# Kernel optimization log

Hardware: AMD Instinct MI355X
Metric: run time of the kernel (lower is better)

## Reference

```python
import jax, jax.numpy as jnp
import numpy as np

SHIFT = 4
MARGIN = 0.15


def _shift_loss(f1, m1, f2, m2):
    # f1,f2: [B,C,H,W] float; m1,m2: [B,1,H,W] bool
    # Original repeats masks to C channels; broadcasting is equivalent,
    # but mask.sum over (1,2,3) then includes a factor of C.
    C = f1.shape[1]
    dists = []
    for i in range(2 * SHIFT + 1):
        off = -SHIFT + i
        f2r = jnp.roll(f2, off, axis=-1)
        m2r = jnp.roll(m2, off, axis=-1)
        mask = m1 & m2r                              # [B,1,H,W]
        diff = jnp.where(mask, f1 - f2r, 0.0)        # broadcast over C
        num = jnp.sum(diff * diff, axis=(1, 2, 3))   # ||.||_2^2
        den = C * jnp.sum(mask, axis=(1, 2, 3)).astype(f1.dtype) + 0.001
        dists.append(num / den)
    return jnp.min(jnp.stack(dists, axis=0), axis=0)  # min over 9 shifts -> [B]


def setup_inputs() -> dict:
    key = jax.random.key(0)
    ka, kp, kn, kma, kmp, kmn = jax.random.split(key, 6)
    B, C, H, W = 64, 16, 32, 512
    a = jax.random.normal(ka, (B, C, H, W), dtype=jnp.float32)
    p = jax.random.normal(kp, (B, C, H, W), dtype=jnp.float32)
    n = jax.random.normal(kn, (B, C, H, W), dtype=jnp.float32)
    ma = jax.random.bernoulli(kma, 0.8, (B, 1, H, W))
    mp = jax.random.bernoulli(kmp, 0.8, (B, 1, H, W))
    mn = jax.random.bernoulli(kmn, 0.8, (B, 1, H, W))
    return {"a": a, "p": p, "n": n, "ma": ma, "mp": mp, "mn": mn}


def reference(a, p, n, ma, mp, mn):
    ap_loss = _shift_loss(a, ma, p, mp)
    an_loss = _shift_loss(a, ma, n, mn)
    loss = jax.nn.relu(ap_loss - an_loss + MARGIN)
    return jnp.mean(loss)
```

## Files before the change

### kernel.cpp

```cpp
#include <hip/hip_runtime.h>

#define NB 64
#define NC 16
#define NH 32
#define NW 512
#define HW (NH * NW)
#define CHW (NC * HW)
#define NOFF 9

#define WS_NUM_AP 0
#define WS_NUM_AN 576
#define WS_CNT_AP 1152
#define WS_CNT_AN 1728
#define WS_FLOATS 2304

__device__ __forceinline__ float wave_sum_f(float v) {
#pragma unroll
    for (int o = 32; o > 0; o >>= 1) v += __shfl_down(v, o, 64);
    return v;
}

__global__ __launch_bounds__(256, 4) void num_kernel(
    const float* __restrict__ a, const float* __restrict__ p,
    const float* __restrict__ n, const int* __restrict__ ma,
    const int* __restrict__ mp, const int* __restrict__ mn,
    float* __restrict__ ws)
{
    const int b    = blockIdx.z;
    const int pair = blockIdx.y & 1;
    const int cg   = blockIdx.y >> 1;
    const int tid  = blockIdx.x * 256 + threadIdx.x;
    const int pos0 = tid * 4;
    const int w0   = pos0 & (NW - 1);
    const int row  = pos0 - w0;
    const int idxm = row + ((w0 - 4) & (NW - 1));
    const int idxp = row + ((w0 + 4) & (NW - 1));

    const int* MA = ma + b * HW;
    const int* M2 = (pair ? mn : mp) + b * HW;
    int4 mav = *(const int4*)(MA + pos0);
    int4 mf0 = *(const int4*)(M2 + idxm);
    int4 mf1 = *(const int4*)(M2 + pos0);
    int4 mf2 = *(const int4*)(M2 + idxp);

    float m1f[4]  = {mav.x ? 1.f : 0.f, mav.y ? 1.f : 0.f,
                     mav.z ? 1.f : 0.f, mav.w ? 1.f : 0.f};
    float m2f[12] = {mf0.x ? 1.f : 0.f, mf0.y ? 1.f : 0.f, mf0.z ? 1.f : 0.f, mf0.w ? 1.f : 0.f,
                     mf1.x ? 1.f : 0.f, mf1.y ? 1.f : 0.f, mf1.z ? 1.f : 0.f, mf1.w ? 1.f : 0.f,
                     mf2.x ? 1.f : 0.f, mf2.y ? 1.f : 0.f, mf2.z ? 1.f : 0.f, mf2.w ? 1.f : 0.f};

    const float* A = a + (size_t)b * CHW + (size_t)cg * 8 * HW;
    const float* F = (pair ? n : p) + (size_t)b * CHW + (size_t)cg * 8 * HW;

    float sa2[4];
    float sf2[12];
    float crS[NOFF];
#pragma unroll
    for (int j = 0; j < 4; ++j) sa2[j] = 0.f;
#pragma unroll
    for (int k = 0; k < 12; ++k) sf2[k] = 0.f;
#pragma unroll
    for (int s = 0; s < NOFF; ++s) crS[s] = 0.f;

#pragma unroll 2
    for (int c = 0; c < 8; ++c) {
        const float* Ac = A + c * HW;
        const float* Fc = F + c * HW;

        float4 av4 = *(const float4*)(Ac + pos0);
        float fb[12];
        *(float4*)&fb[0] = *(const float4*)(Fc + idxm);
        *(float4*)&fb[4] = *(const float4*)(Fc + pos0);
        *(float4*)&fb[8] = *(const float4*)(Fc + idxp);
        float avr[4] = {av4.x, av4.y, av4.z, av4.w};

        float am[4], fm[12];
#pragma unroll
        for (int j = 0; j < 4; ++j) am[j] = avr[j] * m1f[j];
#pragma unroll
        for (int k = 0; k < 12; ++k) fm[k] = fb[k] * m2f[k];

#pragma unroll
        for (int j = 0; j < 4; ++j) sa2[j] = fmaf(am[j], am[j], sa2[j]);
#pragma unroll
        for (int k = 0; k < 12; ++k) sf2[k] = fmaf(fm[k], fm[k], sf2[k]);
#pragma unroll
        for (int s = 0; s < NOFF; ++s) {
#pragma unroll
            for (int j = 0; j < 4; ++j) {
                crS[s] = fmaf(am[j], fm[j + 8 - s], crS[s]);
            }
        }
    }

    float sx[NOFF], cxf[NOFF];
#pragma unroll
    for (int s = 0; s < NOFF; ++s) {
        float t = 0.f, cc = 0.f;
#pragma unroll
        for (int j = 0; j < 4; ++j) {
            const int k = j + 8 - s;
            t  = fmaf(m2f[k], sa2[j], t);
            t  = fmaf(m1f[j], sf2[k], t);
            cc = fmaf(m1f[j], m2f[k], cc);
        }
        sx[s]  = fmaf(-2.f, crS[s], t);
        cxf[s] = cc;
    }

    __shared__ float red[4][20];
    const int lane = threadIdx.x & 63;
    const int wid  = threadIdx.x >> 6;

#pragma unroll
    for (int s = 0; s < NOFF; ++s) sx[s] = wave_sum_f(sx[s]);
    if (cg == 0) {
#pragma unroll
        for (int s = 0; s < NOFF; ++s) cxf[s] = wave_sum_f(cxf[s]);
    }
    if (lane == 0) {
#pragma unroll
        for (int s = 0; s < NOFF; ++s) {
            red[wid][s] = sx[s];
            red[wid][9 + s] = cxf[s];
        }
    }
    __syncthreads();

    float* numws = ws + (pair ? WS_NUM_AN : WS_NUM_AP) + b * NOFF;
    float* cntws = ws + (pair ? WS_CNT_AN : WS_CNT_AP) + b * NOFF;
    const int i = threadIdx.x;
    if (i < 9) {
        float v = red[0][i] + red[1][i] + red[2][i] + red[3][i];
        atomicAdd(numws + i, v);
    } else if (i < 18 && cg == 0) {
        float v = red[0][i] + red[1][i] + red[2][i] + red[3][i];
        atomicAdd(cntws + (i - 9), v);
    }
}

__global__ void finish_kernel(const float* __restrict__ ws, float* __restrict__ out)
{
    const int b = threadIdx.x;
    const float* num_ap = ws + WS_NUM_AP;
    const float* num_an = ws + WS_NUM_AN;
    const float* cnt_ap = ws + WS_CNT_AP;
    const float* cnt_an = ws + WS_CNT_AN;

    float ap = 3.4e38f, an = 3.4e38f;
#pragma unroll
    for (int s = 0; s < NOFF; ++s) {
        ap = fminf(ap, num_ap[b * NOFF + s] / (16.f * cnt_ap[b * NOFF + s] + 0.001f));
        an = fminf(an, num_an[b * NOFF + s] / (16.f * cnt_an[b * NOFF + s] + 0.001f));
    }
    float loss = fmaxf(ap - an + 0.15f, 0.f);
    loss = wave_sum_f(loss);
    if (b == 0) out[0] = loss * (1.0f / 64.f);
}

extern "C" void kernel_launch(void* const* d_in, const int* in_sizes, int n_in,
                              void* d_out, int out_size, void* d_ws, size_t ws_size,
                              hipStream_t stream) {
    const float* a = (const float*)d_in[0];
    const float* p = (const float*)d_in[1];
    const float* n = (const float*)d_in[2];
    const int* ma = (const int*)d_in[3];
    const int* mp = (const int*)d_in[4];
    const int* mn = (const int*)d_in[5];
    float* ws = (float*)d_ws;
    float* out = (float*)d_out;

    hipMemsetAsync(d_ws, 0, WS_FLOATS * sizeof(float), stream);

    num_kernel<<<dim3(16, 4, NB), 256, 0, stream>>>(a, p, n, ma, mp, mn, ws);
    finish_kernel<<<1, 64, 0, stream>>>(ws, out);
}
```

Baseline: 212.9 us.

## Stage shifted feature rows through LDS with double-buffered async global-to-LDS loads

```diff
diff --git a/kernel.cpp b/kernel.cpp
--- a/kernel.cpp
+++ b/kernel.cpp
@@ -18,6 +18,13 @@
 #pragma unroll
     for (int o = 32; o > 0; o >>= 1) v += __shfl_down(v, o, 64);
     return v;
+}
+
+__device__ __forceinline__ void stage16(const float* g, float* lds) {
+    __builtin_amdgcn_global_load_lds(
+        (const __attribute__((address_space(1))) void*)g,
+        (__attribute__((address_space(3))) void*)lds,
+        16, 0, 0);
 }
 
 __global__ __launch_bounds__(256, 4) void num_kernel(
@@ -29,12 +36,17 @@
     const int b    = blockIdx.z;
     const int pair = blockIdx.y & 1;
     const int cg   = blockIdx.y >> 1;
-    const int tid  = blockIdx.x * 256 + threadIdx.x;
-    const int pos0 = tid * 4;
-    const int w0   = pos0 & (NW - 1);
-    const int row  = pos0 - w0;
-    const int idxm = row + ((w0 - 4) & (NW - 1));
-    const int idxp = row + ((w0 + 4) & (NW - 1));
+    const int lane = threadIdx.x & 63;
+    const int wid  = threadIdx.x >> 6;
+
+    const int blockStart = blockIdx.x * 1024;
+    const int lp   = threadIdx.x * 4;
+    const int lrow = lp & ~(NW - 1);
+    const int lw   = lp & (NW - 1);
+    const int pos0 = blockStart + lp;
+    const int grow = pos0 - lw;
+    const int idxm = grow + ((lw - 4) & (NW - 1));
+    const int idxp = grow + ((lw + 4) & (NW - 1));
 
     const int* MA = ma + b * HW;
     const int* M2 = (pair ? mn : mp) + b * HW;
@@ -51,6 +63,11 @@
 
     const float* A = a + (size_t)b * CHW + (size_t)cg * 8 * HW;
     const float* F = (pair ? n : p) + (size_t)b * CHW + (size_t)cg * 8 * HW;
+    const float* AG = A + blockStart;
+    const float* FG = F + blockStart;
+
+    __shared__ float fbuf[2][2][1024];
+    __shared__ float red[4][20];
 
     float sa2[4];
     float sf2[12];
@@ -62,33 +79,53 @@
 #pragma unroll
     for (int s = 0; s < NOFF; ++s) crS[s] = 0.f;
 
-#pragma unroll 2
-    for (int c = 0; c < 8; ++c) {
-        const float* Ac = A + c * HW;
-        const float* Fc = F + c * HW;
-
-        float4 av4 = *(const float4*)(Ac + pos0);
-        float fb[12];
-        *(float4*)&fb[0] = *(const float4*)(Fc + idxm);
-        *(float4*)&fb[4] = *(const float4*)(Fc + pos0);
-        *(float4*)&fb[8] = *(const float4*)(Fc + idxp);
-        float avr[4] = {av4.x, av4.y, av4.z, av4.w};
-
-        float am[4], fm[12];
-#pragma unroll
-        for (int j = 0; j < 4; ++j) am[j] = avr[j] * m1f[j];
-#pragma unroll
-        for (int k = 0; k < 12; ++k) fm[k] = fb[k] * m2f[k];
-
-#pragma unroll
-        for (int j = 0; j < 4; ++j) sa2[j] = fmaf(am[j], am[j], sa2[j]);
-#pragma unroll
-        for (int k = 0; k < 12; ++k) sf2[k] = fmaf(fm[k], fm[k], sf2[k]);
-#pragma unroll
-        for (int s = 0; s < NOFF; ++s) {
-#pragma unroll
-            for (int j = 0; j < 4; ++j) {
-                crS[s] = fmaf(am[j], fm[j + 8 - s], crS[s]);
+    float4 aP[2][2];
+    aP[0][0] = *(const float4*)(AG + 0 * HW);
+    aP[0][1] = *(const float4*)(AG + 1 * HW);
+
+    stage16(FG + 0 * HW + wid * 256 + lane * 4, &fbuf[0][0][wid * 256]);
+    stage16(FG + 1 * HW + wid * 256 + lane * 4, &fbuf[0][1][wid * 256]);
+
+#pragma unroll
+    for (int r = 0; r < 4; ++r) {
+        __syncthreads();
+
+        if (r < 3) {
+            const int c0 = 2 * r + 2;
+            stage16(FG + (c0    ) * HW + wid * 256 + lane * 4, &fbuf[(r + 1) & 1][0][wid * 256]);
+            stage16(FG + (c0 + 1) * HW + wid * 256 + lane * 4, &fbuf[(r + 1) & 1][1][wid * 256]);
+            aP[(r + 1) & 1][0] = *(const float4*)(AG + (c0    ) * HW);
+            aP[(r + 1) & 1][1] = *(const float4*)(AG + (c0 + 1) * HW);
+        }
+
+#pragma unroll
+        for (int q = 0; q < 2; ++q) {
+            const float* fb = &fbuf[r & 1][q][lrow];
+            float4 f0 = *(const float4*)&fb[(lw - 4) & (NW - 1)];
+            float4 f1 = *(const float4*)&fb[lw];
+            float4 f2 = *(const float4*)&fb[(lw + 4) & (NW - 1)];
+            float fbv[12] = {f0.x, f0.y, f0.z, f0.w,
+                             f1.x, f1.y, f1.z, f1.w,
+                             f2.x, f2.y, f2.z, f2.w};
+            float4 a4 = aP[r & 1][q];
+            float avr[4] = {a4.x, a4.y, a4.z, a4.w};
+
+            float am[4], fm[12];
+#pragma unroll
+            for (int j = 0; j < 4; ++j) am[j] = avr[j] * m1f[j];
+#pragma unroll
+            for (int k = 0; k < 12; ++k) fm[k] = fbv[k] * m2f[k];
+
+#pragma unroll
+            for (int j = 0; j < 4; ++j) sa2[j] = fmaf(am[j], am[j], sa2[j]);
+#pragma unroll
+            for (int k = 0; k < 12; ++k) sf2[k] = fmaf(fm[k], fm[k], sf2[k]);
+#pragma unroll
+            for (int s = 0; s < NOFF; ++s) {
+#pragma unroll
+                for (int j = 0; j < 4; ++j) {
+                    crS[s] = fmaf(am[j], fm[j + 8 - s], crS[s]);
+                }
             }
         }
     }
@@ -107,10 +144,6 @@
         sx[s]  = fmaf(-2.f, crS[s], t);
         cxf[s] = cc;
     }
-
-    __shared__ float red[4][20];
-    const int lane = threadIdx.x & 63;
-    const int wid  = threadIdx.x >> 6;
 
 #pragma unroll
     for (int s = 0; s < NOFF; ++s) sx[s] = wave_sum_f(sx[s]);
```

Result: slower. 245.8 us (+15.5%).
